# Performance work log

Hardware: AMD Instinct MI355X
Metric: run time of the kernel (lower is better)

The kernel has to match this reference:

```python
import jax, jax.numpy as jnp
import numpy as np

GAMMA = 2.0
EPS = 1e-06
LAMBDA_DISTANCE = 1.0
LAMBDA_NORMAL = 0.01
LAMBDA_LAPLACIAN = 0.1
CLS = 1


def vertex_normals(v, f, eps=EPS):
    # v: [N,3], f: [F,3] int. Scatter face normals to vertices, then normalize.
    fv = v[f]  # [F,3,3]
    fn = jnp.cross(fv[:, 1] - fv[:, 0], fv[:, 2] - fv[:, 0])  # [F,3]
    vn = jnp.zeros_like(v)
    vn = vn.at[f[:, 0]].add(fn).at[f[:, 1]].add(fn).at[f[:, 2]].add(fn)
    norm = jnp.maximum(jnp.linalg.norm(vn, axis=-1, keepdims=True), eps)
    return vn / norm


def squared_cdist(a, b):
    # [Na,3] x [Nb,3] -> squared euclidean distances [Na,Nb] (clamped >= 0)
    a2 = jnp.sum(a * a, axis=1)[:, None]
    b2 = jnp.sum(b * b, axis=1)[None, :]
    d2 = a2 + b2 - 2.0 * (a @ b.T)
    return jnp.maximum(d2, 0.0)


def sample_binary_targets(label, v, cls=CLS):
    # Nearest-neighbor grid_sample, align_corners=True, padding zeros.
    # grid = 2*v - 1 -> voxel index = round(v * (size-1)); v[:,0]->W, v[:,1]->H, v[:,2]->D.
    D, H, W = label.shape[2], label.shape[3], label.shape[4]
    ix = jnp.round(v[:, 0] * (W - 1)).astype(jnp.int32)
    iy = jnp.round(v[:, 1] * (H - 1)).astype(jnp.int32)
    iz = jnp.round(v[:, 2] * (D - 1)).astype(jnp.int32)
    inb = (ix >= 0) & (ix < W) & (iy >= 0) & (iy < H) & (iz >= 0) & (iz < D)
    ixc = jnp.clip(ix, 0, W - 1)
    iyc = jnp.clip(iy, 0, H - 1)
    izc = jnp.clip(iz, 0, D - 1)
    vals = (label[0, 0, izc, iyc, ixc] == cls).astype(jnp.float32)
    return jnp.where(inb, vals, 0.0)


def spatial_consistency_loss(rel_pos, targets, gamma=GAMMA, eps=EPS):
    p = jnp.clip(rel_pos, eps, 1.0 - eps)
    pos = targets > 0.5
    pc = jnp.sum(pos).astype(p.dtype)
    tot = jnp.asarray(p.shape[0], p.dtype)
    nc = tot - pc
    alpha = nc / (tot + eps)
    lpos = -alpha * jnp.power(1.0 - p, gamma) * jnp.log(p)
    lneg = -(1.0 - alpha) * jnp.power(p, gamma) * jnp.log(1.0 - p)
    return jnp.sum(jnp.where(pos, lpos, lneg)) / (tot + eps)


def laplacian_uniform(v, f):
    # Uniform mesh Laplacian smoothing: || mean(neighbors) - v ||, averaged.
    i = jnp.concatenate([f[:, 0], f[:, 1], f[:, 2], f[:, 1], f[:, 2], f[:, 0]])
    j = jnp.concatenate([f[:, 1], f[:, 2], f[:, 0], f[:, 0], f[:, 1], f[:, 2]])
    nsum = jnp.zeros_like(v).at[i].add(v[j])
    deg = jnp.zeros((v.shape[0],), v.dtype).at[i].add(1.0)
    lap = nsum / jnp.maximum(deg, 1.0)[:, None] - v
    return jnp.mean(jnp.linalg.norm(lap, axis=1))


def loss_forward(pred_vertices, relative_positions, gt_vertices, pred_faces, gt_faces, label):
    gt_v = jax.lax.stop_gradient(gt_vertices)  # gt comes from label volume; detached in original
    gt_normals = vertex_normals(gt_v, gt_faces)
    # spatial (focal-style) loss
    targets = sample_binary_targets(label, pred_vertices)
    spatial = spatial_consistency_loss(relative_positions, targets)
    # chamfer-style squared surface distance
    d2 = squared_cdist(pred_vertices, gt_v)  # [Np,Ng]
    distance = jnp.mean(jnp.min(d2, axis=1)) + jnp.mean(jnp.min(d2, axis=0))
    # normal consistency vs nearest gt vertex
    pred_normals = vertex_normals(pred_vertices, pred_faces)
    nearest = jnp.argmin(d2, axis=1)
    normal = jnp.mean((pred_normals - gt_normals[nearest]) ** 2)
    # uniform laplacian smoothing
    laplacian = laplacian_uniform(pred_vertices, pred_faces)
    total = spatial + LAMBDA_DISTANCE * distance + LAMBDA_NORMAL * normal + LAMBDA_LAPLACIAN * laplacian
    return total


def setup_inputs() -> dict:
    key = jax.random.key(0)
    k1, k2, k3, k4, k5, k6 = jax.random.split(key, 6)
    Np, Ng = 8192, 12000
    pred_vertices = jax.random.uniform(k1, (Np, 3), dtype=jnp.float32)
    relative_positions = jax.random.uniform(k2, (Np,), dtype=jnp.float32)
    gt_vertices = jax.random.uniform(k3, (Ng, 3), dtype=jnp.float32)
    pred_faces = jax.random.randint(k4, (2 * Np, 3), 0, Np, dtype=jnp.int32)
    gt_faces = jax.random.randint(k5, (2 * Ng, 3), 0, Ng, dtype=jnp.int32)
    label = jax.random.randint(k6, (1, 1, 96, 96, 96), 0, 2, dtype=jnp.int32)
    return {"pred_vertices": pred_vertices, "relative_positions": relative_positions,
            "gt_vertices": gt_vertices, "pred_faces": pred_faces,
            "gt_faces": gt_faces, "label": label}


def reference(pred_vertices, relative_positions, gt_vertices, pred_faces, gt_faces, label):
    return loss_forward(pred_vertices, relative_positions, gt_vertices, pred_faces, gt_faces, label)
```

## Files before the change

kernel.cpp:

```cpp
#include <hip/hip_runtime.h>
#include <math.h>

#define NP 8192
#define NG 12000
#define NFP 16384
#define NFG 24000
#define EPSF 1e-6f

#define GR 16
#define NC (GR*GR*GR)
#define HCELL 0.0625f
#define QL 16
#define QPB (256 / QL)
#define PRED_QBLOCKS (NP / QPB)
#define GT_QBLOCKS (NG / QPB)
#define FIN_TOTAL (PRED_QBLOCKS + GT_QBLOCKS)

static constexpr size_t OFF_STARTP = 0;
static constexpr size_t OFF_CURP   = 16640;
static constexpr size_t OFF_STARTG = 33024;
static constexpr size_t OFF_CURG   = 49664;
static constexpr size_t OFF_SORTP  = 66048;
static constexpr size_t OFF_SORTG  = 197120;
static constexpr size_t OFF_GTN    = 389120;
static constexpr size_t OFF_PNN    = 533120;
static constexpr size_t OFF_NSUM   = 631424;
static constexpr size_t OFF_DEG    = 729728;
static constexpr size_t OFF_PART   = 762496;
#define N_ZERO 93344

__device__ __forceinline__ int cell_of(float x) {
    int c = (int)(x * (float)GR);
    return min(max(c, 0), GR - 1);
}

__device__ __forceinline__ void hist_scan(const float* __restrict__ pts, int n,
                                          unsigned* __restrict__ start,
                                          unsigned* __restrict__ cur,
                                          unsigned* h, unsigned* ps) {
    int t = threadIdx.x;
    for (int i = t; i < NC; i += 1024) h[i] = 0u;
    __syncthreads();
    for (int i = t; i < n; i += 1024) {
        int c = (cell_of(pts[3*i+2]) * GR + cell_of(pts[3*i+1])) * GR + cell_of(pts[3*i]);
        atomicAdd(&h[c], 1u);
    }
    __syncthreads();
    unsigned a0 = h[4*t], a1 = h[4*t+1], a2 = h[4*t+2], a3 = h[4*t+3];
    unsigned tsum = a0 + a1 + a2 + a3;
    ps[t] = tsum; __syncthreads();
    for (int off = 1; off < 1024; off <<= 1) {
        unsigned v = (t >= off) ? ps[t - off] : 0u;
        __syncthreads();
        ps[t] += v;
        __syncthreads();
    }
    unsigned ex = ps[t] - tsum;
    h[4*t] = ex; h[4*t+1] = ex + a0; h[4*t+2] = ex + a0 + a1; h[4*t+3] = ex + a0 + a1 + a2;
    __syncthreads();
    for (int i = t; i < NC; i += 1024) { start[i] = h[i]; cur[i] = h[i]; }
    if (t == 0) start[NC] = (unsigned)n;
}

__global__ __launch_bounds__(1024) void build_kernel(const float* __restrict__ pred,
                                                     const float* __restrict__ gt,
                                                     unsigned* __restrict__ startP,
                                                     unsigned* __restrict__ curP,
                                                     unsigned* __restrict__ startG,
                                                     unsigned* __restrict__ curG,
                                                     float* __restrict__ zero) {
    __shared__ unsigned h[NC];
    __shared__ unsigned ps[1024];
    if (blockIdx.x == 0) {
        hist_scan(pred, NP, startP, curP, h, ps);
    } else if (blockIdx.x == 1) {
        hist_scan(gt, NG, startG, curG, h, ps);
    } else {
        int i = (blockIdx.x - 2) * 1024 + threadIdx.x;
        if (i < N_ZERO) zero[i] = 0.0f;
    }
}

#define SCAT_P_BLOCKS 32
#define SCAT_G_BLOCKS 47
#define SCAT_BLOCKS (SCAT_P_BLOCKS + SCAT_G_BLOCKS)
#define FACE_BLOCKS ((NFG + NFP + 255) / 256)
__global__ __launch_bounds__(256) void scatter_faces_kernel(const float* __restrict__ pred,
                                                            const int* __restrict__ pf,
                                                            const float* __restrict__ gt,
                                                            const int* __restrict__ gf,
                                                            unsigned* __restrict__ curP,
                                                            unsigned* __restrict__ curG,
                                                            float4* __restrict__ sortP,
                                                            float4* __restrict__ sortG,
                                                            float* __restrict__ gtn,
                                                            float* __restrict__ pnn,
                                                            float* __restrict__ nsum,
                                                            float* __restrict__ deg) {
    int b = blockIdx.x;
    if (b < SCAT_P_BLOCKS) {
        int i = b * 256 + threadIdx.x;
        float x = pred[3*i], y = pred[3*i+1], z = pred[3*i+2];
        int c = (cell_of(z) * GR + cell_of(y)) * GR + cell_of(x);
        unsigned pos = atomicAdd(&curP[c], 1u);
        sortP[pos] = make_float4(x, y, z, __int_as_float(i));
    } else if (b < SCAT_BLOCKS) {
        int i = (b - SCAT_P_BLOCKS) * 256 + threadIdx.x;
        if (i < NG) {
            float x = gt[3*i], y = gt[3*i+1], z = gt[3*i+2];
            int c = (cell_of(z) * GR + cell_of(y)) * GR + cell_of(x);
            unsigned pos = atomicAdd(&curG[c], 1u);
            sortG[pos] = make_float4(x, y, z, __int_as_float(i));
        }
    } else {
        int t = (b - SCAT_BLOCKS) * 256 + threadIdx.x;
        if (t < NFG) {
            int i0 = gf[3*t], i1 = gf[3*t+1], i2 = gf[3*t+2];
            float ax = gt[3*i0], ay = gt[3*i0+1], az = gt[3*i0+2];
            float bx = gt[3*i1], by = gt[3*i1+1], bz = gt[3*i1+2];
            float cx = gt[3*i2], cy = gt[3*i2+1], cz = gt[3*i2+2];
            float ux = bx-ax, uy = by-ay, uz = bz-az;
            float wx = cx-ax, wy = cy-ay, wz = cz-az;
            float nx = uy*wz - uz*wy, ny = uz*wx - ux*wz, nz = ux*wy - uy*wx;
            atomicAdd(&gtn[3*i0+0], nx); atomicAdd(&gtn[3*i0+1], ny); atomicAdd(&gtn[3*i0+2], nz);
            atomicAdd(&gtn[3*i1+0], nx); atomicAdd(&gtn[3*i1+1], ny); atomicAdd(&gtn[3*i1+2], nz);
            atomicAdd(&gtn[3*i2+0], nx); atomicAdd(&gtn[3*i2+1], ny); atomicAdd(&gtn[3*i2+2], nz);
        } else if (t < NFG + NFP) {
            int u = t - NFG;
            int i0 = pf[3*u], i1 = pf[3*u+1], i2 = pf[3*u+2];
            float ax = pred[3*i0], ay = pred[3*i0+1], az = pred[3*i0+2];
            float bx = pred[3*i1], by = pred[3*i1+1], bz = pred[3*i1+2];
            float cx = pred[3*i2], cy = pred[3*i2+1], cz = pred[3*i2+2];
            float ux = bx-ax, uy = by-ay, uz = bz-az;
            float wx = cx-ax, wy = cy-ay, wz = cz-az;
            float nx = uy*wz - uz*wy, ny = uz*wx - ux*wz, nz = ux*wy - uy*wx;
            atomicAdd(&pnn[3*i0+0], nx); atomicAdd(&pnn[3*i0+1], ny); atomicAdd(&pnn[3*i0+2], nz);
            atomicAdd(&pnn[3*i1+0], nx); atomicAdd(&pnn[3*i1+1], ny); atomicAdd(&pnn[3*i1+2], nz);
            atomicAdd(&pnn[3*i2+0], nx); atomicAdd(&pnn[3*i2+1], ny); atomicAdd(&pnn[3*i2+2], nz);
            atomicAdd(&nsum[3*i0+0], bx+cx); atomicAdd(&nsum[3*i0+1], by+cy); atomicAdd(&nsum[3*i0+2], bz+cz);
            atomicAdd(&nsum[3*i1+0], cx+ax); atomicAdd(&nsum[3*i1+1], cy+ay); atomicAdd(&nsum[3*i1+2], cz+az);
            atomicAdd(&nsum[3*i2+0], ax+bx); atomicAdd(&nsum[3*i2+1], ay+by); atomicAdd(&nsum[3*i2+2], az+bz);
            atomicAdd(&deg[i0], 2.0f); atomicAdd(&deg[i1], 2.0f); atomicAdd(&deg[i2], 2.0f);
        }
    }
}

__device__ __forceinline__ float wave_sum(float x) {
    #pragma unroll
    for (int o = 32; o > 0; o >>= 1) x += __shfl_down(x, o, 64);
    return x;
}

__device__ __forceinline__ unsigned long long u64min(unsigned long long a,
                                                     unsigned long long b) {
    return a < b ? a : b;
}

__device__ __forceinline__ unsigned long long group_nn(int lane,
                                                       float px, float py, float pz,
                                                       const float4* __restrict__ S,
                                                       const unsigned* __restrict__ cstart) {
    int cx = cell_of(px), cy = cell_of(py), cz = cell_of(pz);
    unsigned long long best = 0xFFFFFFFFFFFFFFFFULL;
    for (int r = 1; ; ++r) {
        int w = 2 * r + 1;
        int nrows = w * w;
        int x0 = max(cx - r, 0), x1 = min(cx + r, GR - 1);
        unsigned long long lb = 0xFFFFFFFFFFFFFFFFULL;
        for (int k = lane; k < nrows; k += QL) {
            int z = cz + k / w - r, y = cy + k % w - r;
            if (z >= 0 && z < GR && y >= 0 && y < GR) {
                int rowbase = (z * GR + y) * GR;
                unsigned s0 = cstart[rowbase + x0];
                unsigned s1 = cstart[rowbase + x1 + 1];
                for (unsigned t = s0; t < s1; ++t) {
                    float4 q = S[t];
                    float ddx = px - q.x, ddy = py - q.y, ddz = pz - q.z;
                    float d2 = fmaf(ddx, ddx, fmaf(ddy, ddy, ddz*ddz));
                    unsigned long long key =
                        ((unsigned long long)__float_as_uint(d2) << 32) |
                        (unsigned)__float_as_int(q.w);
                    lb = u64min(lb, key);
                }
            }
        }
        best = u64min(best, lb);
        #pragma unroll
        for (int m = 1; m < QL; m <<= 1)
            best = u64min(best, (unsigned long long)__shfl_xor((long long)best, m, 64));
        bool covered = (cx - r <= 0) & (cx + r >= GR - 1) &
                       (cy - r <= 0) & (cy + r >= GR - 1) &
                       (cz - r <= 0) & (cz + r >= GR - 1);
        if (covered) break;
        float blo = 1.0e30f;
        if (cx - r > 0)      blo = fminf(blo, px - (float)(cx - r) * HCELL);
        if (cx + r < GR - 1) blo = fminf(blo, (float)(cx + r + 1) * HCELL - px);
        if (cy - r > 0)      blo = fminf(blo, py - (float)(cy - r) * HCELL);
        if (cy + r < GR - 1) blo = fminf(blo, (float)(cy + r + 1) * HCELL - py);
        if (cz - r > 0)      blo = fminf(blo, pz - (float)(cz - r) * HCELL);
        if (cz + r < GR - 1) blo = fminf(blo, (float)(cz + r + 1) * HCELL - pz);
        float bd2 = __uint_as_float((unsigned)(best >> 32));
        if (bd2 <= blo * blo) break;
    }
    return best;
}

__global__ __launch_bounds__(256) void query_kernel(const float* __restrict__ relpos,
                                                    const int* __restrict__ label,
                                                    const float4* __restrict__ sortP,
                                                    const float4* __restrict__ sortG,
                                                    const unsigned* __restrict__ startP,
                                                    const unsigned* __restrict__ startG,
                                                    const float* __restrict__ pnn,
                                                    const float* __restrict__ gtn,
                                                    const float* __restrict__ nsum,
                                                    const float* __restrict__ deg,
                                                    float* __restrict__ partial) {
    __shared__ float bsum[6];
    if (threadIdx.x < 6) bsum[threadIdx.x] = 0.0f;
    __syncthreads();
    int lane = threadIdx.x & (QL - 1);
    int group = threadIdx.x >> 4;
    if (blockIdx.x < PRED_QBLOCKS) {
        int qid = blockIdx.x * QPB + group;
        float4 P = sortP[qid];
        float px = P.x, py = P.y, pz = P.z;
        unsigned long long key = group_nn(lane, px, py, pz, sortG, startG);

        float r0 = 0.f, r1 = 0.f, r2 = 0.f, r3 = 0.f, r4 = 0.f, r5 = 0.f;
        if (lane == 0) {
            int v = __float_as_int(P.w);
            float dmin = __uint_as_float((unsigned)(key >> 32));
            int nearest = (int)(unsigned)(key & 0xffffffffu);

            float ax = pnn[3*v], ay = pnn[3*v+1], az = pnn[3*v+2];
            float an = fmaxf(sqrtf(ax*ax + ay*ay + az*az), EPSF);
            float gx = gtn[3*nearest], gy = gtn[3*nearest+1], gz = gtn[3*nearest+2];
            float gn = fmaxf(sqrtf(gx*gx + gy*gy + gz*gz), EPSF);
            float nx = ax/an - gx/gn, ny = ay/an - gy/gn, nz = az/an - gz/gn;
            float sse = nx*nx + ny*ny + nz*nz;

            float d = fmaxf(deg[v], 1.0f);
            float lx = nsum[3*v]/d - px, ly = nsum[3*v+1]/d - py, lz = nsum[3*v+2]/d - pz;
            float lapn = sqrtf(lx*lx + ly*ly + lz*lz);

            int ix = (int)rintf(px * 95.0f), iy = (int)rintf(py * 95.0f), iz = (int)rintf(pz * 95.0f);
            bool inb = (ix >= 0) & (ix < 96) & (iy >= 0) & (iy < 96) & (iz >= 0) & (iz < 96);
            int ixc = min(max(ix, 0), 95), iyc = min(max(iy, 0), 95), izc = min(max(iz, 0), 95);
            bool pos = inb && (label[(izc*96 + iyc)*96 + ixc] == 1);

            float p = fminf(fmaxf(relpos[v], EPSF), 1.0f - EPSF);
            float om = 1.0f - p;
            float pcnt = 0.0f, sx = 0.0f, sy = 0.0f;
            if (pos) { pcnt = 1.0f; sx = om*om*logf(p); }
            else     { sy = p*p*logf(om); }

            r0 = dmin; r1 = sse; r2 = lapn; r3 = pcnt; r4 = sx; r5 = sy;
        }
        r0 = wave_sum(r0); r1 = wave_sum(r1); r2 = wave_sum(r2);
        r3 = wave_sum(r3); r4 = wave_sum(r4); r5 = wave_sum(r5);
        if ((threadIdx.x & 63) == 0) {
            atomicAdd(&bsum[0], r0); atomicAdd(&bsum[1], r1);
            atomicAdd(&bsum[2], r2); atomicAdd(&bsum[3], r3);
            atomicAdd(&bsum[4], r4); atomicAdd(&bsum[5], r5);
        }
        __syncthreads();
        if (threadIdx.x < 6)
            partial[(size_t)blockIdx.x * 8 + threadIdx.x] = bsum[threadIdx.x];
    } else {
        int qid = (blockIdx.x - PRED_QBLOCKS) * QPB + group;
        float4 Q = sortG[qid];
        unsigned long long key = group_nn(lane, Q.x, Q.y, Q.z, sortP, startP);
        float val = (lane == 0) ? __uint_as_float((unsigned)(key >> 32)) : 0.0f;
        float r = wave_sum(val);
        if ((threadIdx.x & 63) == 0) atomicAdd(&bsum[0], r);
        __syncthreads();
        if (threadIdx.x == 0)
            partial[(size_t)blockIdx.x * 8] = bsum[0];
    }
}

__global__ __launch_bounds__(256) void combine_kernel(const float* __restrict__ partial,
                                                      float* __restrict__ out) {
    float s0=0.f, s1=0.f, s2=0.f, s3=0.f, s4=0.f, s5=0.f, s6=0.f;
    for (int r = threadIdx.x; r < FIN_TOTAL; r += 256) {
        const float* p = partial + (size_t)r * 8;
        if (r < PRED_QBLOCKS) {
            s0 += p[0]; s1 += p[1]; s2 += p[2];
            s3 += p[3]; s4 += p[4]; s5 += p[5];
        } else {
            s6 += p[0];
        }
    }
    s0 = wave_sum(s0); s1 = wave_sum(s1); s2 = wave_sum(s2); s3 = wave_sum(s3);
    s4 = wave_sum(s4); s5 = wave_sum(s5); s6 = wave_sum(s6);
    __shared__ float acc[7];
    if (threadIdx.x < 7) acc[threadIdx.x] = 0.0f;
    __syncthreads();
    if ((threadIdx.x & 63) == 0) {
        atomicAdd(&acc[0], s0); atomicAdd(&acc[1], s1); atomicAdd(&acc[2], s2);
        atomicAdd(&acc[3], s3); atomicAdd(&acc[4], s4); atomicAdd(&acc[5], s5);
        atomicAdd(&acc[6], s6);
    }
    __syncthreads();
    if (threadIdx.x == 0) {
        float sum_row = acc[0], sse = acc[1], lap = acc[2];
        float pc = acc[3], SX = acc[4], SY = acc[5], sum_col = acc[6];
        float tot = (float)NP;
        float alpha = (tot - pc) / (tot + EPSF);
        float spatial = (-alpha * SX - (1.0f - alpha) * SY) / (tot + EPSF);
        float distance = sum_row / (float)NP + sum_col / (float)NG;
        float normal = sse / (float)(NP * 3);
        float lapm = lap / (float)NP;
        out[0] = spatial + 1.0f * distance + 0.01f * normal + 0.1f * lapm;
    }
}

extern "C" void kernel_launch(void* const* d_in, const int* in_sizes, int n_in,
                              void* d_out, int out_size, void* d_ws, size_t ws_size,
                              hipStream_t stream) {
    const float* pred   = (const float*)d_in[0];
    const float* relpos = (const float*)d_in[1];
    const float* gt     = (const float*)d_in[2];
    const int*   pfaces = (const int*)d_in[3];
    const int*   gfaces = (const int*)d_in[4];
    const int*   label  = (const int*)d_in[5];
    float* out = (float*)d_out;

    char* ws = (char*)d_ws;
    unsigned* startP  = (unsigned*)(ws + OFF_STARTP);
    unsigned* curP    = (unsigned*)(ws + OFF_CURP);
    unsigned* startG  = (unsigned*)(ws + OFF_STARTG);
    unsigned* curG    = (unsigned*)(ws + OFF_CURG);
    float4*   sortP   = (float4*)(ws + OFF_SORTP);
    float4*   sortG   = (float4*)(ws + OFF_SORTG);
    float*    gtn     = (float*)(ws + OFF_GTN);
    float*    pnn     = (float*)(ws + OFF_PNN);
    float*    nsum    = (float*)(ws + OFF_NSUM);
    float*    deg     = (float*)(ws + OFF_DEG);
    float*    partial = (float*)(ws + OFF_PART);

    int zero_blocks = (N_ZERO + 1023) / 1024;
    hipLaunchKernelGGL(build_kernel, dim3(2 + zero_blocks), dim3(1024), 0, stream,
                       pred, gt, startP, curP, startG, curG, gtn);
    hipLaunchKernelGGL(scatter_faces_kernel, dim3(SCAT_BLOCKS + FACE_BLOCKS), dim3(256), 0, stream,
                       pred, pfaces, gt, gfaces, curP, curG, sortP, sortG,
                       gtn, pnn, nsum, deg);
    hipLaunchKernelGGL(query_kernel, dim3(FIN_TOTAL), dim3(256), 0, stream,
                       relpos, label, sortP, sortG, startP, startG,
                       pnn, gtn, nsum, deg, partial);
    hipLaunchKernelGGL(combine_kernel, dim3(1), dim3(256), 0, stream, partial, out);
}
```

Baseline: 118.0 us.

## Fuse point scatter into cell build, overlap face normals with NN queries

Each cloud's single build block now also scatters its points into cell-sorted order using LDS atomics. The prefix scan switches from a barrier-heavy shared-memory loop to wave shuffles. Face-normal and Laplacian scatter-adds run in the same launch as the nearest-neighbour queries, and per-vertex loss terms move to a finish kernel that folds the final combine in through a last-block-done counter. The aim is fewer launches and overlap of the atomic face work with the queries. The trade-off is that scattering each cloud from one block is less parallel, and the nearest index now takes an extra global round trip.

```diff
diff --git a/kernel.cpp b/kernel.cpp
--- a/kernel.cpp
+++ b/kernel.cpp
@@ -14,31 +14,34 @@
 #define QPB (256 / QL)
 #define PRED_QBLOCKS (NP / QPB)
 #define GT_QBLOCKS (NG / QPB)
-#define FIN_TOTAL (PRED_QBLOCKS + GT_QBLOCKS)
+#define FACE_BLOCKS ((NFG + NFP + 255) / 256)
+#define QF_BLOCKS (PRED_QBLOCKS + GT_QBLOCKS + FACE_BLOCKS)
+#define FIN_BLOCKS (NP / 256)
 
 static constexpr size_t OFF_STARTP = 0;
-static constexpr size_t OFF_CURP   = 16640;
-static constexpr size_t OFF_STARTG = 33024;
-static constexpr size_t OFF_CURG   = 49664;
-static constexpr size_t OFF_SORTP  = 66048;
-static constexpr size_t OFF_SORTG  = 197120;
-static constexpr size_t OFF_GTN    = 389120;
-static constexpr size_t OFF_PNN    = 533120;
-static constexpr size_t OFF_NSUM   = 631424;
-static constexpr size_t OFF_DEG    = 729728;
-static constexpr size_t OFF_PART   = 762496;
-#define N_ZERO 93344
+static constexpr size_t OFF_STARTG = 16640;
+static constexpr size_t OFF_SORTP  = 33280;
+static constexpr size_t OFF_SORTG  = 164352;
+static constexpr size_t OFF_GTN    = 356352;
+static constexpr size_t OFF_PNN    = 500352;
+static constexpr size_t OFF_NSUM   = 598656;
+static constexpr size_t OFF_DEG    = 696960;
+static constexpr size_t OFF_NEAR   = 729728;
+static constexpr size_t OFF_ACCUM  = 762496;
+static constexpr size_t OFF_DONE   = 762528;
+#define N_ZERO 101545
 
 __device__ __forceinline__ int cell_of(float x) {
     int c = (int)(x * (float)GR);
     return min(max(c, 0), GR - 1);
 }
 
-__device__ __forceinline__ void hist_scan(const float* __restrict__ pts, int n,
-                                          unsigned* __restrict__ start,
-                                          unsigned* __restrict__ cur,
-                                          unsigned* h, unsigned* ps) {
+__device__ __forceinline__ void build_cells(const float* __restrict__ pts, int n,
+                                            unsigned* __restrict__ start,
+                                            float4* __restrict__ sorted,
+                                            unsigned* h, unsigned* wsum) {
     int t = threadIdx.x;
+    int lane = t & 63, wid = t >> 6;
     for (int i = t; i < NC; i += 1024) h[i] = 0u;
     __syncthreads();
     for (int i = t; i < n; i += 1024) {
@@ -48,100 +51,54 @@
     __syncthreads();
     unsigned a0 = h[4*t], a1 = h[4*t+1], a2 = h[4*t+2], a3 = h[4*t+3];
     unsigned tsum = a0 + a1 + a2 + a3;
-    ps[t] = tsum; __syncthreads();
-    for (int off = 1; off < 1024; off <<= 1) {
-        unsigned v = (t >= off) ? ps[t - off] : 0u;
-        __syncthreads();
-        ps[t] += v;
-        __syncthreads();
-    }
-    unsigned ex = ps[t] - tsum;
-    h[4*t] = ex; h[4*t+1] = ex + a0; h[4*t+2] = ex + a0 + a1; h[4*t+3] = ex + a0 + a1 + a2;
-    __syncthreads();
-    for (int i = t; i < NC; i += 1024) { start[i] = h[i]; cur[i] = h[i]; }
+    unsigned x = tsum;
+    #pragma unroll
+    for (int off = 1; off < 64; off <<= 1) {
+        unsigned y = __shfl_up(x, off, 64);
+        if (lane >= off) x += y;
+    }
+    if (lane == 63) wsum[wid] = x;
+    __syncthreads();
+    if (t < 16) {
+        unsigned w = wsum[t];
+        #pragma unroll
+        for (int off = 1; off < 16; off <<= 1) {
+            unsigned y = __shfl_up(w, off, 64);
+            if (t >= off) w += y;
+        }
+        wsum[t] = w;
+    }
+    __syncthreads();
+    unsigned base = (wid ? wsum[wid-1] : 0u) + (x - tsum);
+    unsigned e0 = base, e1 = base + a0, e2 = base + a0 + a1, e3 = base + a0 + a1 + a2;
+    start[4*t] = e0; start[4*t+1] = e1; start[4*t+2] = e2; start[4*t+3] = e3;
+    h[4*t] = e0; h[4*t+1] = e1; h[4*t+2] = e2; h[4*t+3] = e3;
+    __syncthreads();
+    for (int i = t; i < n; i += 1024) {
+        float px = pts[3*i], py = pts[3*i+1], pz = pts[3*i+2];
+        int c = (cell_of(pz) * GR + cell_of(py)) * GR + cell_of(px);
+        unsigned pos = atomicAdd(&h[c], 1u);
+        sorted[pos] = make_float4(px, py, pz, __int_as_float(i));
+    }
     if (t == 0) start[NC] = (unsigned)n;
 }
 
 __global__ __launch_bounds__(1024) void build_kernel(const float* __restrict__ pred,
                                                      const float* __restrict__ gt,
                                                      unsigned* __restrict__ startP,
-                                                     unsigned* __restrict__ curP,
                                                      unsigned* __restrict__ startG,
-                                                     unsigned* __restrict__ curG,
+                                                     float4* __restrict__ sortP,
+                                                     float4* __restrict__ sortG,
                                                      float* __restrict__ zero) {
     __shared__ unsigned h[NC];
-    __shared__ unsigned ps[1024];
+    __shared__ unsigned wsum[16];
     if (blockIdx.x == 0) {
-        hist_scan(pred, NP, startP, curP, h, ps);
+        build_cells(pred, NP, startP, sortP, h, wsum);
     } else if (blockIdx.x == 1) {
-        hist_scan(gt, NG, startG, curG, h, ps);
+        build_cells(gt, NG, startG, sortG, h, wsum);
     } else {
         int i = (blockIdx.x - 2) * 1024 + threadIdx.x;
         if (i < N_ZERO) zero[i] = 0.0f;
-    }
-}
-
-#define SCAT_P_BLOCKS 32
-#define SCAT_G_BLOCKS 47
-#define SCAT_BLOCKS (SCAT_P_BLOCKS + SCAT_G_BLOCKS)
-#define FACE_BLOCKS ((NFG + NFP + 255) / 256)
-__global__ __launch_bounds__(256) void scatter_faces_kernel(const float* __restrict__ pred,
-                                                            const int* __restrict__ pf,
-                                                            const float* __restrict__ gt,
-                                                            const int* __restrict__ gf,
-                                                            unsigned* __restrict__ curP,
-                                                            unsigned* __restrict__ curG,
-                                                            float4* __restrict__ sortP,
-                                                            float4* __restrict__ sortG,
-                                                            float* __restrict__ gtn,
-                                                            float* __restrict__ pnn,
-                                                            float* __restrict__ nsum,
-                                                            float* __restrict__ deg) {
-    int b = blockIdx.x;
-    if (b < SCAT_P_BLOCKS) {
-        int i = b * 256 + threadIdx.x;
-        float x = pred[3*i], y = pred[3*i+1], z = pred[3*i+2];
-        int c = (cell_of(z) * GR + cell_of(y)) * GR + cell_of(x);
-        unsigned pos = atomicAdd(&curP[c], 1u);
-        sortP[pos] = make_float4(x, y, z, __int_as_float(i));
-    } else if (b < SCAT_BLOCKS) {
-        int i = (b - SCAT_P_BLOCKS) * 256 + threadIdx.x;
-        if (i < NG) {
-            float x = gt[3*i], y = gt[3*i+1], z = gt[3*i+2];
-            int c = (cell_of(z) * GR + cell_of(y)) * GR + cell_of(x);
-            unsigned pos = atomicAdd(&curG[c], 1u);
-            sortG[pos] = make_float4(x, y, z, __int_as_float(i));
-        }
-    } else {
-        int t = (b - SCAT_BLOCKS) * 256 + threadIdx.x;
-        if (t < NFG) {
-            int i0 = gf[3*t], i1 = gf[3*t+1], i2 = gf[3*t+2];
-            float ax = gt[3*i0], ay = gt[3*i0+1], az = gt[3*i0+2];
-            float bx = gt[3*i1], by = gt[3*i1+1], bz = gt[3*i1+2];
-            float cx = gt[3*i2], cy = gt[3*i2+1], cz = gt[3*i2+2];
-            float ux = bx-ax, uy = by-ay, uz = bz-az;
-            float wx = cx-ax, wy = cy-ay, wz = cz-az;
-            float nx = uy*wz - uz*wy, ny = uz*wx - ux*wz, nz = ux*wy - uy*wx;
-            atomicAdd(&gtn[3*i0+0], nx); atomicAdd(&gtn[3*i0+1], ny); atomicAdd(&gtn[3*i0+2], nz);
-            atomicAdd(&gtn[3*i1+0], nx); atomicAdd(&gtn[3*i1+1], ny); atomicAdd(&gtn[3*i1+2], nz);
-            atomicAdd(&gtn[3*i2+0], nx); atomicAdd(&gtn[3*i2+1], ny); atomicAdd(&gtn[3*i2+2], nz);
-        } else if (t < NFG + NFP) {
-            int u = t - NFG;
-            int i0 = pf[3*u], i1 = pf[3*u+1], i2 = pf[3*u+2];
-            float ax = pred[3*i0], ay = pred[3*i0+1], az = pred[3*i0+2];
-            float bx = pred[3*i1], by = pred[3*i1+1], bz = pred[3*i1+2];
-            float cx = pred[3*i2], cy = pred[3*i2+1], cz = pred[3*i2+2];
-            float ux = bx-ax, uy = by-ay, uz = bz-az;
-            float wx = cx-ax, wy = cy-ay, wz = cz-az;
-            float nx = uy*wz - uz*wy, ny = uz*wx - ux*wz, nz = ux*wy - uy*wx;
-            atomicAdd(&pnn[3*i0+0], nx); atomicAdd(&pnn[3*i0+1], ny); atomicAdd(&pnn[3*i0+2], nz);
-            atomicAdd(&pnn[3*i1+0], nx); atomicAdd(&pnn[3*i1+1], ny); atomicAdd(&pnn[3*i1+2], nz);
-            atomicAdd(&pnn[3*i2+0], nx); atomicAdd(&pnn[3*i2+1], ny); atomicAdd(&pnn[3*i2+2], nz);
-            atomicAdd(&nsum[3*i0+0], bx+cx); atomicAdd(&nsum[3*i0+1], by+cy); atomicAdd(&nsum[3*i0+2], bz+cz);
-            atomicAdd(&nsum[3*i1+0], cx+ax); atomicAdd(&nsum[3*i1+1], cy+ay); atomicAdd(&nsum[3*i1+2], cz+az);
-            atomicAdd(&nsum[3*i2+0], ax+bx); atomicAdd(&nsum[3*i2+1], ay+by); atomicAdd(&nsum[3*i2+2], az+bz);
-            atomicAdd(&deg[i0], 2.0f); atomicAdd(&deg[i1], 2.0f); atomicAdd(&deg[i2], 2.0f);
-        }
     }
 }
 
@@ -205,113 +162,153 @@
     return best;
 }
 
-__global__ __launch_bounds__(256) void query_kernel(const float* __restrict__ relpos,
-                                                    const int* __restrict__ label,
-                                                    const float4* __restrict__ sortP,
-                                                    const float4* __restrict__ sortG,
-                                                    const unsigned* __restrict__ startP,
-                                                    const unsigned* __restrict__ startG,
-                                                    const float* __restrict__ pnn,
-                                                    const float* __restrict__ gtn,
-                                                    const float* __restrict__ nsum,
-                                                    const float* __restrict__ deg,
-                                                    float* __restrict__ partial) {
-    __shared__ float bsum[6];
-    if (threadIdx.x < 6) bsum[threadIdx.x] = 0.0f;
-    __syncthreads();
-    int lane = threadIdx.x & (QL - 1);
-    int group = threadIdx.x >> 4;
-    if (blockIdx.x < PRED_QBLOCKS) {
-        int qid = blockIdx.x * QPB + group;
-        float4 P = sortP[qid];
-        float px = P.x, py = P.y, pz = P.z;
-        unsigned long long key = group_nn(lane, px, py, pz, sortG, startG);
-
-        float r0 = 0.f, r1 = 0.f, r2 = 0.f, r3 = 0.f, r4 = 0.f, r5 = 0.f;
-        if (lane == 0) {
-            int v = __float_as_int(P.w);
-            float dmin = __uint_as_float((unsigned)(key >> 32));
-            int nearest = (int)(unsigned)(key & 0xffffffffu);
-
-            float ax = pnn[3*v], ay = pnn[3*v+1], az = pnn[3*v+2];
-            float an = fmaxf(sqrtf(ax*ax + ay*ay + az*az), EPSF);
-            float gx = gtn[3*nearest], gy = gtn[3*nearest+1], gz = gtn[3*nearest+2];
-            float gn = fmaxf(sqrtf(gx*gx + gy*gy + gz*gz), EPSF);
-            float nx = ax/an - gx/gn, ny = ay/an - gy/gn, nz = az/an - gz/gn;
-            float sse = nx*nx + ny*ny + nz*nz;
-
-            float d = fmaxf(deg[v], 1.0f);
-            float lx = nsum[3*v]/d - px, ly = nsum[3*v+1]/d - py, lz = nsum[3*v+2]/d - pz;
-            float lapn = sqrtf(lx*lx + ly*ly + lz*lz);
-
-            int ix = (int)rintf(px * 95.0f), iy = (int)rintf(py * 95.0f), iz = (int)rintf(pz * 95.0f);
-            bool inb = (ix >= 0) & (ix < 96) & (iy >= 0) & (iy < 96) & (iz >= 0) & (iz < 96);
-            int ixc = min(max(ix, 0), 95), iyc = min(max(iy, 0), 95), izc = min(max(iz, 0), 95);
-            bool pos = inb && (label[(izc*96 + iyc)*96 + ixc] == 1);
-
-            float p = fminf(fmaxf(relpos[v], EPSF), 1.0f - EPSF);
-            float om = 1.0f - p;
-            float pcnt = 0.0f, sx = 0.0f, sy = 0.0f;
-            if (pos) { pcnt = 1.0f; sx = om*om*logf(p); }
-            else     { sy = p*p*logf(om); }
-
-            r0 = dmin; r1 = sse; r2 = lapn; r3 = pcnt; r4 = sx; r5 = sy;
+__global__ __launch_bounds__(256) void query_face_kernel(const float* __restrict__ pred,
+                                                         const int* __restrict__ pf,
+                                                         const float* __restrict__ gt,
+                                                         const int* __restrict__ gf,
+                                                         const float4* __restrict__ sortP,
+                                                         const float4* __restrict__ sortG,
+                                                         const unsigned* __restrict__ startP,
+                                                         const unsigned* __restrict__ startG,
+                                                         float* __restrict__ gtn,
+                                                         float* __restrict__ pnn,
+                                                         float* __restrict__ nsum,
+                                                         float* __restrict__ deg,
+                                                         int* __restrict__ nearestIdx,
+                                                         float* __restrict__ accum) {
+    int b = blockIdx.x;
+    if (b < PRED_QBLOCKS + GT_QBLOCKS) {
+        __shared__ float bs;
+        if (threadIdx.x == 0) bs = 0.0f;
+        __syncthreads();
+        int lane = threadIdx.x & (QL - 1);
+        int group = threadIdx.x >> 4;
+        float r0 = 0.0f;
+        if (b < PRED_QBLOCKS) {
+            int qid = b * QPB + group;
+            float4 P = sortP[qid];
+            unsigned long long key = group_nn(lane, P.x, P.y, P.z, sortG, startG);
+            if (lane == 0) {
+                int v = __float_as_int(P.w);
+                nearestIdx[v] = (int)(unsigned)(key & 0xffffffffu);
+                r0 = __uint_as_float((unsigned)(key >> 32));
+            }
+        } else {
+            int qid = (b - PRED_QBLOCKS) * QPB + group;
+            float4 Q = sortG[qid];
+            unsigned long long key = group_nn(lane, Q.x, Q.y, Q.z, sortP, startP);
+            if (lane == 0) r0 = __uint_as_float((unsigned)(key >> 32));
         }
-        r0 = wave_sum(r0); r1 = wave_sum(r1); r2 = wave_sum(r2);
-        r3 = wave_sum(r3); r4 = wave_sum(r4); r5 = wave_sum(r5);
-        if ((threadIdx.x & 63) == 0) {
-            atomicAdd(&bsum[0], r0); atomicAdd(&bsum[1], r1);
-            atomicAdd(&bsum[2], r2); atomicAdd(&bsum[3], r3);
-            atomicAdd(&bsum[4], r4); atomicAdd(&bsum[5], r5);
-        }
-        __syncthreads();
-        if (threadIdx.x < 6)
-            partial[(size_t)blockIdx.x * 8 + threadIdx.x] = bsum[threadIdx.x];
-    } else {
-        int qid = (blockIdx.x - PRED_QBLOCKS) * QPB + group;
-        float4 Q = sortG[qid];
-        unsigned long long key = group_nn(lane, Q.x, Q.y, Q.z, sortP, startP);
-        float val = (lane == 0) ? __uint_as_float((unsigned)(key >> 32)) : 0.0f;
-        float r = wave_sum(val);
-        if ((threadIdx.x & 63) == 0) atomicAdd(&bsum[0], r);
+        r0 = wave_sum(r0);
+        if ((threadIdx.x & 63) == 0) atomicAdd(&bs, r0);
         __syncthreads();
         if (threadIdx.x == 0)
-            partial[(size_t)blockIdx.x * 8] = bsum[0];
-    }
-}
-
-__global__ __launch_bounds__(256) void combine_kernel(const float* __restrict__ partial,
-                                                      float* __restrict__ out) {
-    float s0=0.f, s1=0.f, s2=0.f, s3=0.f, s4=0.f, s5=0.f, s6=0.f;
-    for (int r = threadIdx.x; r < FIN_TOTAL; r += 256) {
-        const float* p = partial + (size_t)r * 8;
-        if (r < PRED_QBLOCKS) {
-            s0 += p[0]; s1 += p[1]; s2 += p[2];
-            s3 += p[3]; s4 += p[4]; s5 += p[5];
-        } else {
-            s6 += p[0];
+            atomicAdd(&accum[(b < PRED_QBLOCKS) ? 0 : 6], bs);
+    } else {
+        int t = (b - PRED_QBLOCKS - GT_QBLOCKS) * 256 + threadIdx.x;
+        if (t < NFG) {
+            int i0 = gf[3*t], i1 = gf[3*t+1], i2 = gf[3*t+2];
+            float ax = gt[3*i0], ay = gt[3*i0+1], az = gt[3*i0+2];
+            float bx = gt[3*i1], by = gt[3*i1+1], bz = gt[3*i1+2];
+            float cx = gt[3*i2], cy = gt[3*i2+1], cz = gt[3*i2+2];
+            float ux = bx-ax, uy = by-ay, uz = bz-az;
+            float wx = cx-ax, wy = cy-ay, wz = cz-az;
+            float nx = uy*wz - uz*wy, ny = uz*wx - ux*wz, nz = ux*wy - uy*wx;
+            atomicAdd(&gtn[3*i0+0], nx); atomicAdd(&gtn[3*i0+1], ny); atomicAdd(&gtn[3*i0+2], nz);
+            atomicAdd(&gtn[3*i1+0], nx); atomicAdd(&gtn[3*i1+1], ny); atomicAdd(&gtn[3*i1+2], nz);
+            atomicAdd(&gtn[3*i2+0], nx); atomicAdd(&gtn[3*i2+1], ny); atomicAdd(&gtn[3*i2+2], nz);
+        } else if (t < NFG + NFP) {
+            int u = t - NFG;
+            int i0 = pf[3*u], i1 = pf[3*u+1], i2 = pf[3*u+2];
+            float ax = pred[3*i0], ay = pred[3*i0+1], az = pred[3*i0+2];
+            float bx = pred[3*i1], by = pred[3*i1+1], bz = pred[3*i1+2];
+            float cx = pred[3*i2], cy = pred[3*i2+1], cz = pred[3*i2+2];
+            float ux = bx-ax, uy = by-ay, uz = bz-az;
+            float wx = cx-ax, wy = cy-ay, wz = cz-az;
+            float nx = uy*wz - uz*wy, ny = uz*wx - ux*wz, nz = ux*wy - uy*wx;
+            atomicAdd(&pnn[3*i0+0], nx); atomicAdd(&pnn[3*i0+1], ny); atomicAdd(&pnn[3*i0+2], nz);
+            atomicAdd(&pnn[3*i1+0], nx); atomicAdd(&pnn[3*i1+1], ny); atomicAdd(&pnn[3*i1+2], nz);
+            atomicAdd(&pnn[3*i2+0], nx); atomicAdd(&pnn[3*i2+1], ny); atomicAdd(&pnn[3*i2+2], nz);
+            atomicAdd(&nsum[3*i0+0], bx+cx); atomicAdd(&nsum[3*i0+1], by+cy); atomicAdd(&nsum[3*i0+2], bz+cz);
+            atomicAdd(&nsum[3*i1+0], cx+ax); atomicAdd(&nsum[3*i1+1], cy+ay); atomicAdd(&nsum[3*i1+2], cz+az);
+            atomicAdd(&nsum[3*i2+0], ax+bx); atomicAdd(&nsum[3*i2+1], ay+by); atomicAdd(&nsum[3*i2+2], az+bz);
+            atomicAdd(&deg[i0], 2.0f); atomicAdd(&deg[i1], 2.0f); atomicAdd(&deg[i2], 2.0f);
         }
     }
-    s0 = wave_sum(s0); s1 = wave_sum(s1); s2 = wave_sum(s2); s3 = wave_sum(s3);
-    s4 = wave_sum(s4); s5 = wave_sum(s5); s6 = wave_sum(s6);
-    __shared__ float acc[7];
-    if (threadIdx.x < 7) acc[threadIdx.x] = 0.0f;
+}
+
+__global__ __launch_bounds__(256) void finish_kernel(const float* __restrict__ pred,
+                                                     const float* __restrict__ relpos,
+                                                     const int* __restrict__ label,
+                                                     const float* __restrict__ pnn,
+                                                     const float* __restrict__ gtn,
+                                                     const float* __restrict__ nsum,
+                                                     const float* __restrict__ deg,
+                                                     const int* __restrict__ nearestIdx,
+                                                     float* __restrict__ accum,
+                                                     unsigned* __restrict__ done,
+                                                     float* __restrict__ out) {
+    int v = blockIdx.x * 256 + threadIdx.x;
+    float px = pred[3*v], py = pred[3*v+1], pz = pred[3*v+2];
+    int nearest = nearestIdx[v];
+
+    float ax = pnn[3*v], ay = pnn[3*v+1], az = pnn[3*v+2];
+    float an = fmaxf(sqrtf(ax*ax + ay*ay + az*az), EPSF);
+    float gx = gtn[3*nearest], gy = gtn[3*nearest+1], gz = gtn[3*nearest+2];
+    float gn = fmaxf(sqrtf(gx*gx + gy*gy + gz*gz), EPSF);
+    float nx = ax/an - gx/gn, ny = ay/an - gy/gn, nz = az/an - gz/gn;
+    float sse = nx*nx + ny*ny + nz*nz;
+
+    float d = fmaxf(deg[v], 1.0f);
+    float lx = nsum[3*v]/d - px, ly = nsum[3*v+1]/d - py, lz = nsum[3*v+2]/d - pz;
+    float lapn = sqrtf(lx*lx + ly*ly + lz*lz);
+
+    int ix = (int)rintf(px * 95.0f), iy = (int)rintf(py * 95.0f), iz = (int)rintf(pz * 95.0f);
+    bool inb = (ix >= 0) & (ix < 96) & (iy >= 0) & (iy < 96) & (iz >= 0) & (iz < 96);
+    int ixc = min(max(ix, 0), 95), iyc = min(max(iy, 0), 95), izc = min(max(iz, 0), 95);
+    bool pos = inb && (label[(izc*96 + iyc)*96 + ixc] == 1);
+
+    float p = fminf(fmaxf(relpos[v], EPSF), 1.0f - EPSF);
+    float om = 1.0f - p;
+    float pcnt = 0.0f, sx = 0.0f, sy = 0.0f;
+    if (pos) { pcnt = 1.0f; sx = om*om*logf(p); }
+    else     { sy = p*p*logf(om); }
+
+    float r1 = wave_sum(sse), r2 = wave_sum(lapn), r3 = wave_sum(pcnt);
+    float r4 = wave_sum(sx),  r5 = wave_sum(sy);
+    __shared__ float bsum[5];
+    __shared__ bool isLast;
+    if (threadIdx.x < 5) bsum[threadIdx.x] = 0.0f;
     __syncthreads();
     if ((threadIdx.x & 63) == 0) {
-        atomicAdd(&acc[0], s0); atomicAdd(&acc[1], s1); atomicAdd(&acc[2], s2);
-        atomicAdd(&acc[3], s3); atomicAdd(&acc[4], s4); atomicAdd(&acc[5], s5);
-        atomicAdd(&acc[6], s6);
+        atomicAdd(&bsum[0], r1); atomicAdd(&bsum[1], r2); atomicAdd(&bsum[2], r3);
+        atomicAdd(&bsum[3], r4); atomicAdd(&bsum[4], r5);
     }
     __syncthreads();
     if (threadIdx.x == 0) {
-        float sum_row = acc[0], sse = acc[1], lap = acc[2];
-        float pc = acc[3], SX = acc[4], SY = acc[5], sum_col = acc[6];
+        atomicAdd(&accum[1], bsum[0]); atomicAdd(&accum[2], bsum[1]);
+        atomicAdd(&accum[3], bsum[2]); atomicAdd(&accum[4], bsum[3]);
+        atomicAdd(&accum[5], bsum[4]);
+        __threadfence();
+        unsigned prev = atomicAdd(done, 1u);
+        isLast = (prev == FIN_BLOCKS - 1);
+    }
+    __syncthreads();
+    if (isLast && threadIdx.x == 0) {
+        __threadfence();
+        float sum_row = __hip_atomic_load(&accum[0], __ATOMIC_RELAXED, __HIP_MEMORY_SCOPE_AGENT);
+        float sse_t   = __hip_atomic_load(&accum[1], __ATOMIC_RELAXED, __HIP_MEMORY_SCOPE_AGENT);
+        float lap_t   = __hip_atomic_load(&accum[2], __ATOMIC_RELAXED, __HIP_MEMORY_SCOPE_AGENT);
+        float pc      = __hip_atomic_load(&accum[3], __ATOMIC_RELAXED, __HIP_MEMORY_SCOPE_AGENT);
+        float SX      = __hip_atomic_load(&accum[4], __ATOMIC_RELAXED, __HIP_MEMORY_SCOPE_AGENT);
+        float SY      = __hip_atomic_load(&accum[5], __ATOMIC_RELAXED, __HIP_MEMORY_SCOPE_AGENT);
+        float sum_col = __hip_atomic_load(&accum[6], __ATOMIC_RELAXED, __HIP_MEMORY_SCOPE_AGENT);
         float tot = (float)NP;
         float alpha = (tot - pc) / (tot + EPSF);
         float spatial = (-alpha * SX - (1.0f - alpha) * SY) / (tot + EPSF);
         float distance = sum_row / (float)NP + sum_col / (float)NG;
-        float normal = sse / (float)(NP * 3);
-        float lapm = lap / (float)NP;
+        float normal = sse_t / (float)(NP * 3);
+        float lapm = lap_t / (float)NP;
         out[0] = spatial + 1.0f * distance + 0.01f * normal + 0.1f * lapm;
     }
 }
@@ -329,25 +326,24 @@
 
     char* ws = (char*)d_ws;
     unsigned* startP  = (unsigned*)(ws + OFF_STARTP);
-    unsigned* curP    = (unsigned*)(ws + OFF_CURP);
     unsigned* startG  = (unsigned*)(ws + OFF_STARTG);
-    unsigned* curG    = (unsigned*)(ws + OFF_CURG);
     float4*   sortP   = (float4*)(ws + OFF_SORTP);
     float4*   sortG   = (float4*)(ws + OFF_SORTG);
     float*    gtn     = (float*)(ws + OFF_GTN);
     float*    pnn     = (float*)(ws + OFF_PNN);
     float*    nsum    = (float*)(ws + OFF_NSUM);
     float*    deg     = (float*)(ws + OFF_DEG);
-    float*    partial = (float*)(ws + OFF_PART);
+    int*      nearest = (int*)(ws + OFF_NEAR);
+    float*    accum   = (float*)(ws + OFF_ACCUM);
+    unsigned* done    = (unsigned*)(ws + OFF_DONE);
 
     int zero_blocks = (N_ZERO + 1023) / 1024;
     hipLaunchKernelGGL(build_kernel, dim3(2 + zero_blocks), dim3(1024), 0, stream,
-                       pred, gt, startP, curP, startG, curG, gtn);
-    hipLaunchKernelGGL(scatter_faces_kernel, dim3(SCAT_BLOCKS + FACE_BLOCKS), dim3(256), 0, stream,
-                       pred, pfaces, gt, gfaces, curP, curG, sortP, sortG,
-                       gtn, pnn, nsum, deg);
-    hipLaunchKernelGGL(query_kernel, dim3(FIN_TOTAL), dim3(256), 0, stream,
-                       relpos, label, sortP, sortG, startP, startG,
-                       pnn, gtn, nsum, deg, partial);
-    hipLaunchKernelGGL(combine_kernel, dim3(1), dim3(256), 0, stream, partial, out);
-}
+                       pred, gt, startP, startG, sortP, sortG, (float*)(ws + OFF_GTN));
+    hipLaunchKernelGGL(query_face_kernel, dim3(QF_BLOCKS), dim3(256), 0, stream,
+                       pred, pfaces, gt, gfaces, sortP, sortG, startP, startG,
+                       gtn, pnn, nsum, deg, nearest, accum);
+    hipLaunchKernelGGL(finish_kernel, dim3(FIN_BLOCKS), dim3(256), 0, stream,
+                       pred, relpos, label, pnn, gtn, nsum, deg, nearest,
+                       accum, done, out);
+}
```

Measured after the change: 124.7 us. +5.6%, slower.
